# Kernel tuning notes

Hardware: AMD Instinct MI355X
Metric: run time of the kernel (lower is better)

## Reference

```python
import jax, jax.numpy as jnp
import numpy as np

B, D_IN, D_H, K, M = 4096, 512, 128, 16, 1250
N_GENES = K * M  # 20000


def setup_inputs() -> dict:
    key = jax.random.key(0)
    k_z, k_w1, k_w2 = jax.random.split(key, 3)
    z = jax.random.normal(k_z, (B, D_IN), dtype=jnp.float32)
    # Stacked parameters for the K identical-shape HydraHeads
    # (Linear(d_in, d_hidden) -> ReLU -> Linear(d_hidden, m_k)).
    W1 = jax.random.normal(k_w1, (K, D_IN, D_H), dtype=jnp.float32) / np.sqrt(D_IN)
    b1 = jnp.zeros((K, D_H), dtype=jnp.float32)
    W2 = jax.random.normal(k_w2, (K, D_H, M), dtype=jnp.float32) / np.sqrt(D_H)
    b2 = jnp.zeros((K, M), dtype=jnp.float32)
    # Strided canonical-order partition: head k owns genes k, k+K, k+2K, ...
    idx = jnp.arange(N_GENES, dtype=jnp.int32).reshape(M, K).T  # (K, M)
    return {"z": z, "W1": W1, "b1": b1, "W2": W2, "b2": b2, "idx": idx}


def reference(z, W1, b1, W2, b2, idx):
    # K small MLP heads, batched as one einsum pair instead of a Python loop.
    h = jax.nn.relu(jnp.einsum('bd,kdh->kbh', z, W1) + b1[:, None, :])   # (K, B, H)
    per_head = jnp.einsum('kbh,khm->kbm', h, W2) + b2[:, None, :]        # (K, B, M)
    # Scatter reassembly into registry-canonical order: full[:, idx[k]] = per_head[k]
    flat_idx = idx.reshape(-1)                                            # (K*M,)
    flat_heads = jnp.transpose(per_head, (1, 0, 2)).reshape(z.shape[0], K * M)
    full = jnp.zeros((z.shape[0], N_GENES), dtype=per_head.dtype)
    full = full.at[:, flat_idx].set(flat_heads)
    return full, per_head
```

## Files before the change

### kernel.cpp

```cpp
#include <hip/hip_runtime.h>


#define DEV static __device__ __forceinline__

typedef __attribute__((ext_vector_type(8))) short bf16x8;
typedef __attribute__((ext_vector_type(4))) float f32x4;
typedef __attribute__((ext_vector_type(4))) short s16x4;

constexpr int B = 4096, DIN = 512, DH = 128, K = 16, M = 1250, NG = K * M;
constexpr int MT = 32;
constexpr int NMT = (M + MT - 1) / MT;
constexpr int LDS_S = 516;

DEV unsigned short f2bf(float x) {
  unsigned u = __builtin_bit_cast(unsigned, x);
  u += 0x7FFFu + ((u >> 16) & 1u);
  return (unsigned short)(u >> 16);
}
DEV float bf2f(unsigned short b) {
  return __builtin_bit_cast(float, (unsigned)b << 16);
}
DEV void split_bf16(float x, short& hi, short& lo) {
  unsigned short h = f2bf(x);
  hi = (short)h;
  lo = (short)f2bf(x - bf2f(h));
}


__global__ __launch_bounds__(256)
void convert_all(const float* __restrict__ z, const float* __restrict__ w1,
                 const float* __restrict__ w2,
                 short* __restrict__ zhi, short* __restrict__ zlo,
                 short* __restrict__ w1hi, short* __restrict__ w1lo,
                 short* __restrict__ w2hi, short* __restrict__ w2lo) {
  const int g = blockIdx.x;
  if (g < 2048) {
    const int i = g * 256 + threadIdx.x;
    const float4 v = ((const float4*)z)[i];
    float vv[4] = {v.x, v.y, v.z, v.w};
    s16x4 h, l;
#pragma unroll
    for (int j = 0; j < 4; ++j) {
      unsigned short a = f2bf(vv[j]);
      h[j] = (short)a;
      l[j] = (short)f2bf(vv[j] - bf2f(a));
    }
    ((s16x4*)zhi)[i] = h;
    ((s16x4*)zlo)[i] = l;
  } else if (g < 6144) {
    const int n = (g - 2048) * 256 + threadIdx.x;
    const int d = n & (DIN - 1);
    const int h = (n >> 9) & (DH - 1);
    const int k = n >> 16;
    split_bf16(w1[(k * DIN + d) * DH + h], w1hi[n], w1lo[n]);
  } else {
    const int n = (g - 6144) * 256 + threadIdx.x;
    const int h = n & (DH - 1);
    const int t = n >> 7;
    const int m = t % M;
    const int k = t / M;
    split_bf16(w2[(k * DH + h) * M + m], w2hi[n], w2lo[n]);
  }
}


__global__ __launch_bounds__(256)
void gemm1(const short* __restrict__ zhi, const short* __restrict__ zlo,
           const short* __restrict__ w1hi, const short* __restrict__ w1lo,
           const float* __restrict__ b1,
           short* __restrict__ hhi, short* __restrict__ hlo) {
  const int lane = threadIdx.x & 63, wave = threadIdx.x >> 6;
  const int lr = lane & 15, lg = lane >> 4;
  const int g = blockIdx.x;
  const int w = (g & 7) * 128 + (g >> 3);
  const int k = w >> 6;
  const int b0 = (w & 63) * 64;
  const int c0 = wave * 32;

  f32x4 acc[4][2] = {};
  const short* w1hk = w1hi + k * DH * DIN;
  const short* w1lk = w1lo + k * DH * DIN;

  for (int kc = 0; kc < DIN; kc += 32) {
    const int ko = kc + lg * 8;
    bf16x8 bh[2], bl[2];
#pragma unroll
    for (int j = 0; j < 2; ++j) {
      const int off = (c0 + j * 16 + lr) * DIN + ko;
      bh[j] = *(const bf16x8*)(w1hk + off);
      bl[j] = *(const bf16x8*)(w1lk + off);
    }
#pragma unroll
    for (int i = 0; i < 4; ++i) {
      const int off = (b0 + i * 16 + lr) * DIN + ko;
      const bf16x8 ah = *(const bf16x8*)(zhi + off);
      const bf16x8 al = *(const bf16x8*)(zlo + off);
#pragma unroll
      for (int j = 0; j < 2; ++j) {
        acc[i][j] = __builtin_amdgcn_mfma_f32_16x16x32_bf16(ah, bh[j], acc[i][j], 0, 0, 0);
        acc[i][j] = __builtin_amdgcn_mfma_f32_16x16x32_bf16(ah, bl[j], acc[i][j], 0, 0, 0);
        acc[i][j] = __builtin_amdgcn_mfma_f32_16x16x32_bf16(al, bh[j], acc[i][j], 0, 0, 0);
      }
    }
  }

#pragma unroll
  for (int i = 0; i < 4; ++i) {
#pragma unroll
    for (int j = 0; j < 2; ++j) {
      const int col = c0 + j * 16 + lr;
      const float bias = b1[k * DH + col];
#pragma unroll
      for (int r = 0; r < 4; ++r) {
        const int row = b0 + i * 16 + lg * 4 + r;
        float v = acc[i][j][r] + bias;
        v = fmaxf(v, 0.f);
        short hi, lo;
        split_bf16(v, hi, lo);
        const int o = (k * B + row) * DH + col;
        hhi[o] = hi;
        hlo[o] = lo;
      }
    }
  }
}


__global__ __launch_bounds__(512)
void gemm2(const short* __restrict__ hhi, const short* __restrict__ hlo,
           const short* __restrict__ w2hi, const short* __restrict__ w2lo,
           const float* __restrict__ b2,
           float* __restrict__ full, float* __restrict__ ph) {
  const int tid = threadIdx.x;
  const int lane = tid & 63, wave = tid >> 6;
  const int lr = lane & 15, lg = lane >> 4;
  const int hgrp = wave & 3;
  const int mgrp = wave >> 2;
  const int g = blockIdx.x;
  const int w = (g & 7) * 320 + (g >> 3);
  const int bt = w / NMT;
  const int mt = w % NMT;
  const int b0 = bt * 64;
  const int m0 = mt * MT;
  const int mloc = mgrp * 16 + lr;
  const int mi = m0 + mloc;
  const int mc = mi < M ? mi : M - 1;
  const int khg = hgrp * 4;

  __shared__ __align__(16) float lds[16 * LDS_S];

  f32x4 acc[4][4] = {};

#pragma unroll
  for (int hk = 0; hk < 4; ++hk) {
    const int kh = khg + hk;
    const short* hh = hhi + ((long)(kh * B + b0)) * DH;
    const short* hl = hlo + ((long)(kh * B + b0)) * DH;
    const short* w2h = w2hi + (kh * M + mc) * DH;
    const short* w2l = w2lo + (kh * M + mc) * DH;
#pragma unroll
    for (int kc = 0; kc < DH; kc += 32) {
      const int ko = kc + lg * 8;
      const bf16x8 bh = *(const bf16x8*)(w2h + ko);
      const bf16x8 bl = *(const bf16x8*)(w2l + ko);
#pragma unroll
      for (int i = 0; i < 4; ++i) {
        const int offa = (i * 16 + lr) * DH + ko;
        const bf16x8 ah = *(const bf16x8*)(hh + offa);
        const bf16x8 al = *(const bf16x8*)(hl + offa);
        acc[hk][i] = __builtin_amdgcn_mfma_f32_16x16x32_bf16(ah, bh, acc[hk][i], 0, 0, 0);
        acc[hk][i] = __builtin_amdgcn_mfma_f32_16x16x32_bf16(ah, bl, acc[hk][i], 0, 0, 0);
        acc[hk][i] = __builtin_amdgcn_mfma_f32_16x16x32_bf16(al, bh, acc[hk][i], 0, 0, 0);
      }
    }
  }

  float bias[4];
#pragma unroll
  for (int hk = 0; hk < 4; ++hk) bias[hk] = b2[(khg + hk) * M + mc];

  const int Mrem = (M - m0 < MT) ? (M - m0) : MT;
  const int nf4 = Mrem * 4;
  const int wslot = (khg >> 2) + 0;

#pragma unroll
  for (int q = 0; q < 4; ++q) {
    __syncthreads();
#pragma unroll
    for (int r = 0; r < 4; ++r) {
      const int rowl = lg * 4 + r;
      f32x4 v;
#pragma unroll
      for (int hk = 0; hk < 4; ++hk) v[hk] = acc[hk][q][r] + bias[hk];
      const int slot = (wslot + mloc) & 3;
      *(f32x4*)&lds[rowl * LDS_S + mloc * 16 + slot * 4] = v;
      if (mi < M) {
        const int row = b0 + q * 16 + rowl;
        __builtin_nontemporal_store(v[0], &ph[((khg + 0) * B + row) * M + mi]);
        __builtin_nontemporal_store(v[1], &ph[((khg + 1) * B + row) * M + mi]);
        __builtin_nontemporal_store(v[2], &ph[((khg + 2) * B + row) * M + mi]);
        __builtin_nontemporal_store(v[3], &ph[((khg + 3) * B + row) * M + mi]);
      }
    }
    __syncthreads();
#pragma unroll
    for (int it = 0; it < 4; ++it) {
      const int f4id = it * 512 + tid;
      const int rowl = f4id >> 7;
      const int c4 = f4id & 127;
      if (c4 < nf4) {
        const int mg = c4 >> 2, s = c4 & 3;
        const int slot = (s + mg) & 3;
        const f32x4 v = *(const f32x4*)&lds[rowl * LDS_S + mg * 16 + slot * 4];
        __builtin_nontemporal_store(
            v, (f32x4*)&full[(b0 + q * 16 + rowl) * NG + m0 * 16 + c4 * 4]);
      }
    }
  }
}


extern "C" void kernel_launch(void* const* d_in, const int* in_sizes, int n_in,
                              void* d_out, int out_size, void* d_ws, size_t ws_size,
                              hipStream_t stream) {
  const float* z  = (const float*)d_in[0];
  const float* W1 = (const float*)d_in[1];
  const float* b1 = (const float*)d_in[2];
  const float* W2 = (const float*)d_in[3];
  const float* b2 = (const float*)d_in[4];

  short* ws = (short*)d_ws;
  const int ZN  = B * DIN;
  const int W1N = K * DIN * DH;
  const int W2N = K * DH * M;
  const int HN  = K * B * DH;
  short* zhi  = ws;           short* zlo  = zhi + ZN;
  short* w1hi = zlo + ZN;     short* w1lo = w1hi + W1N;
  short* w2hi = w1lo + W1N;   short* w2lo = w2hi + W2N;
  short* hhi  = w2lo + W2N;   short* hlo  = hhi + HN;

  float* full = (float*)d_out;
  float* ph   = full + (long)B * NG;

  convert_all<<<16144, 256, 0, stream>>>(z, W1, W2, zhi, zlo, w1hi, w1lo, w2hi, w2lo);
  gemm1<<<64 * K, 256, 0, stream>>>(zhi, zlo, w1hi, w1lo, b1, hhi, hlo);
  gemm2<<<NMT * 64, 512, 0, stream>>>(hhi, hlo, w2hi, w2lo, b2, full, ph);
}
```

Measured before the change: 1.246 ms.

## Stage gemm2 operands through double-buffered LDS with direct global-to-LDS loads

gemm2 now walks the 16 heads sequentially, using global_load_lds to copy swizzled H and W2 tiles into a double-buffered LDS ring. Each stage is prefetched while the MFMAs of the previous stage run, replacing per-lane direct global loads. The wave decomposition changes from head-groups to batch-quarters by M halves, so each wave holds 16 accumulators. The block mapping also becomes M-tile-major. This adds a large dynamic LDS footprint and more barriers, which may limit occupancy, and drops nontemporal stores for the per-head output.

After: 1.050 ms. 15.7% less time.

```diff
diff --git a/kernel.cpp b/kernel.cpp
--- a/kernel.cpp
+++ b/kernel.cpp
@@ -6,11 +6,15 @@
 typedef __attribute__((ext_vector_type(8))) short bf16x8;
 typedef __attribute__((ext_vector_type(4))) float f32x4;
 typedef __attribute__((ext_vector_type(4))) short s16x4;
+typedef unsigned int u32;
 
 constexpr int B = 4096, DIN = 512, DH = 128, K = 16, M = 1250, NG = K * M;
-constexpr int MT = 32;
-constexpr int NMT = (M + MT - 1) / MT;
+constexpr int MT = 32, NMT = 40;
 constexpr int LDS_S = 516;
+constexpr int HBUF = 0;
+constexpr int WBUF = 65536;
+constexpr int PANEL = 98304;
+constexpr int LDS_TOTAL = PANEL + 16 * LDS_S * 4;
 
 DEV unsigned short f2bf(float x) {
   unsigned u = __builtin_bit_cast(unsigned, x);
@@ -24,6 +28,11 @@
   unsigned short h = f2bf(x);
   hi = (short)h;
   lo = (short)f2bf(x - bf2f(h));
+}
+DEV void dma16(const void* g, void* l) {
+  __builtin_amdgcn_global_load_lds(
+      (const __attribute__((address_space(1))) u32*)g,
+      (__attribute__((address_space(3))) u32*)l, 16, 0, 0);
 }
 
 
@@ -126,94 +135,155 @@
 }
 
 
-__global__ __launch_bounds__(512)
+__global__ __launch_bounds__(512, 2)
 void gemm2(const short* __restrict__ hhi, const short* __restrict__ hlo,
            const short* __restrict__ w2hi, const short* __restrict__ w2lo,
            const float* __restrict__ b2,
            float* __restrict__ full, float* __restrict__ ph) {
+  extern __shared__ char smem[];
   const int tid = threadIdx.x;
   const int lane = tid & 63, wave = tid >> 6;
   const int lr = lane & 15, lg = lane >> 4;
-  const int hgrp = wave & 3;
-  const int mgrp = wave >> 2;
+  const int bq = wave >> 1, mg = wave & 1;
   const int g = blockIdx.x;
   const int w = (g & 7) * 320 + (g >> 3);
-  const int bt = w / NMT;
-  const int mt = w % NMT;
-  const int b0 = bt * 64;
-  const int m0 = mt * MT;
-  const int mloc = mgrp * 16 + lr;
+  const int mt = w / 64;
+  const int bt = w % 64;
+  const int b0 = bt * 64, m0 = mt * MT;
+
+  const short* gp[6];
+  int ls0[6], ls1[6];
+  long stride[6];
+#pragma unroll
+  for (int c6 = 0; c6 < 6; ++c6) {
+    const int id = wave + c6 * 8;
+    if (id < 16) {
+      const int c = id;
+      const int row = c * 4 + (lane >> 4);
+      const int sg = (lane & 15) ^ (row & 7);
+      gp[c6] = hhi + (long)(b0 + row) * DH + sg * 8;
+      ls0[c6] = HBUF + c * 1024;
+      ls1[c6] = HBUF + 32768 + c * 1024;
+      stride[c6] = (long)B * DH;
+    } else if (id < 32) {
+      const int c = id - 16;
+      const int row = c * 4 + (lane >> 4);
+      const int sg = (lane & 15) ^ (row & 7);
+      gp[c6] = hlo + (long)(b0 + row) * DH + sg * 8;
+      ls0[c6] = HBUF + 16384 + c * 1024;
+      ls1[c6] = HBUF + 32768 + 16384 + c * 1024;
+      stride[c6] = (long)B * DH;
+    } else if (id < 40) {
+      const int c = id - 32;
+      const int row = c * 4 + (lane >> 4);
+      const int sg = (lane & 15) ^ (row & 7);
+      gp[c6] = w2hi + (long)(m0 + row) * DH + sg * 8;
+      ls0[c6] = WBUF + c * 1024;
+      ls1[c6] = WBUF + 16384 + c * 1024;
+      stride[c6] = (long)M * DH;
+    } else {
+      const int c = id - 40;
+      const int row = c * 4 + (lane >> 4);
+      const int sg = (lane & 15) ^ (row & 7);
+      gp[c6] = w2lo + (long)(m0 + row) * DH + sg * 8;
+      ls0[c6] = WBUF + 8192 + c * 1024;
+      ls1[c6] = WBUF + 16384 + 8192 + c * 1024;
+      stride[c6] = (long)M * DH;
+    }
+  }
+
+#define ISSUE(PAR)                                                  \
+  do {                                                              \
+    _Pragma("unroll") for (int c6 = 0; c6 < 6; ++c6)                \
+        dma16(gp[c6], smem + ((PAR) ? ls1[c6] : ls0[c6]));          \
+  } while (0)
+#define ADV()                                                       \
+  do {                                                              \
+    _Pragma("unroll") for (int c6 = 0; c6 < 6; ++c6)                \
+        gp[c6] += stride[c6];                                       \
+  } while (0)
+
+  f32x4 acc[16] = {};
+  const int arow = bq * 16 + lr;
+  const int mrow = mg * 16 + lr;
+
+  ISSUE(0);
+#pragma unroll
+  for (int p = 0; p < 16; ++p) {
+    if (p < 15) {
+      ADV();
+      if ((p + 1) & 1) ISSUE(1); else ISSUE(0);
+      asm volatile("s_waitcnt vmcnt(6)" ::: "memory");
+    } else {
+      asm volatile("s_waitcnt vmcnt(0)" ::: "memory");
+    }
+    __builtin_amdgcn_sched_barrier(0);
+    __builtin_amdgcn_s_barrier();
+    __builtin_amdgcn_sched_barrier(0);
+    const char* hb = smem + HBUF + ((p & 1) ? 32768 : 0);
+    const char* wb = smem + WBUF + ((p & 1) ? 16384 : 0);
+#pragma unroll
+    for (int s = 0; s < 4; ++s) {
+      const int gx = (((s * 4 + lg) ^ (lr & 7))) * 16;
+      const bf16x8 ah = *(const bf16x8*)(hb + arow * 256 + gx);
+      const bf16x8 al = *(const bf16x8*)(hb + 16384 + arow * 256 + gx);
+      const bf16x8 bh = *(const bf16x8*)(wb + mrow * 256 + gx);
+      const bf16x8 bl = *(const bf16x8*)(wb + 8192 + mrow * 256 + gx);
+      acc[p] = __builtin_amdgcn_mfma_f32_16x16x32_bf16(ah, bh, acc[p], 0, 0, 0);
+      acc[p] = __builtin_amdgcn_mfma_f32_16x16x32_bf16(ah, bl, acc[p], 0, 0, 0);
+      acc[p] = __builtin_amdgcn_mfma_f32_16x16x32_bf16(al, bh, acc[p], 0, 0, 0);
+    }
+    __builtin_amdgcn_sched_barrier(0);
+    __builtin_amdgcn_s_barrier();
+    __builtin_amdgcn_sched_barrier(0);
+  }
+#undef ISSUE
+#undef ADV
+
+  float* panel = (float*)(smem + PANEL);
+  const int mloc = mg * 16 + lr;
   const int mi = m0 + mloc;
-  const int mc = mi < M ? mi : M - 1;
-  const int khg = hgrp * 4;
-
-  __shared__ __align__(16) float lds[16 * LDS_S];
-
-  f32x4 acc[4][4] = {};
-
-#pragma unroll
-  for (int hk = 0; hk < 4; ++hk) {
-    const int kh = khg + hk;
-    const short* hh = hhi + ((long)(kh * B + b0)) * DH;
-    const short* hl = hlo + ((long)(kh * B + b0)) * DH;
-    const short* w2h = w2hi + (kh * M + mc) * DH;
-    const short* w2l = w2lo + (kh * M + mc) * DH;
-#pragma unroll
-    for (int kc = 0; kc < DH; kc += 32) {
-      const int ko = kc + lg * 8;
-      const bf16x8 bh = *(const bf16x8*)(w2h + ko);
-      const bf16x8 bl = *(const bf16x8*)(w2l + ko);
-#pragma unroll
-      for (int i = 0; i < 4; ++i) {
-        const int offa = (i * 16 + lr) * DH + ko;
-        const bf16x8 ah = *(const bf16x8*)(hh + offa);
-        const bf16x8 al = *(const bf16x8*)(hl + offa);
-        acc[hk][i] = __builtin_amdgcn_mfma_f32_16x16x32_bf16(ah, bh, acc[hk][i], 0, 0, 0);
-        acc[hk][i] = __builtin_amdgcn_mfma_f32_16x16x32_bf16(ah, bl, acc[hk][i], 0, 0, 0);
-        acc[hk][i] = __builtin_amdgcn_mfma_f32_16x16x32_bf16(al, bh, acc[hk][i], 0, 0, 0);
-      }
-    }
-  }
-
-  float bias[4];
-#pragma unroll
-  for (int hk = 0; hk < 4; ++hk) bias[hk] = b2[(khg + hk) * M + mc];
-
+  const int mc2 = mi < M ? mi : M - 1;
+  float bias[16];
+#pragma unroll
+  for (int kh = 0; kh < 16; ++kh) bias[kh] = b2[kh * M + mc2];
   const int Mrem = (M - m0 < MT) ? (M - m0) : MT;
   const int nf4 = Mrem * 4;
-  const int wslot = (khg >> 2) + 0;
 
 #pragma unroll
   for (int q = 0; q < 4; ++q) {
     __syncthreads();
-#pragma unroll
-    for (int r = 0; r < 4; ++r) {
-      const int rowl = lg * 4 + r;
-      f32x4 v;
-#pragma unroll
-      for (int hk = 0; hk < 4; ++hk) v[hk] = acc[hk][q][r] + bias[hk];
-      const int slot = (wslot + mloc) & 3;
-      *(f32x4*)&lds[rowl * LDS_S + mloc * 16 + slot * 4] = v;
-      if (mi < M) {
-        const int row = b0 + q * 16 + rowl;
-        __builtin_nontemporal_store(v[0], &ph[((khg + 0) * B + row) * M + mi]);
-        __builtin_nontemporal_store(v[1], &ph[((khg + 1) * B + row) * M + mi]);
-        __builtin_nontemporal_store(v[2], &ph[((khg + 2) * B + row) * M + mi]);
-        __builtin_nontemporal_store(v[3], &ph[((khg + 3) * B + row) * M + mi]);
+    if (bq == q) {
+#pragma unroll
+      for (int r = 0; r < 4; ++r) {
+        const int rowl = lg * 4 + r;
+        const int grow = b0 + q * 16 + rowl;
+#pragma unroll
+        for (int hg = 0; hg < 4; ++hg) {
+          f32x4 v;
+#pragma unroll
+          for (int j = 0; j < 4; ++j) v[j] = acc[hg * 4 + j][r] + bias[hg * 4 + j];
+          const int slot = (hg + (mloc >> 1)) & 3;
+          *(f32x4*)&panel[rowl * LDS_S + mloc * 16 + slot * 4] = v;
+          if (mi < M) {
+#pragma unroll
+            for (int j = 0; j < 4; ++j)
+              ph[((long)(hg * 4 + j) * B + grow) * M + mi] = v[j];
+          }
+        }
       }
     }
     __syncthreads();
 #pragma unroll
     for (int it = 0; it < 4; ++it) {
       const int f4id = it * 512 + tid;
-      const int rowl = f4id >> 7;
-      const int c4 = f4id & 127;
+      const int rowl = f4id >> 7, c4 = f4id & 127;
       if (c4 < nf4) {
-        const int mg = c4 >> 2, s = c4 & 3;
-        const int slot = (s + mg) & 3;
-        const f32x4 v = *(const f32x4*)&lds[rowl * LDS_S + mg * 16 + slot * 4];
+        const int pm = c4 >> 2, hg = c4 & 3;
+        const int slot = (hg + (pm >> 1)) & 3;
+        const f32x4 v = *(const f32x4*)&panel[rowl * LDS_S + pm * 16 + slot * 4];
         __builtin_nontemporal_store(
-            v, (f32x4*)&full[(b0 + q * 16 + rowl) * NG + m0 * 16 + c4 * 4]);
+            v, (f32x4*)&full[(long)(b0 + q * 16 + rowl) * NG + m0 * 16 + c4 * 4]);
       }
     }
   }
@@ -242,7 +312,10 @@
   float* full = (float*)d_out;
   float* ph   = full + (long)B * NG;
 
+  hipFuncSetAttribute((const void*)gemm2,
+                      hipFuncAttributeMaxDynamicSharedMemorySize, LDS_TOTAL);
+
   convert_all<<<16144, 256, 0, stream>>>(z, W1, W2, zhi, zlo, w1hi, w1lo, w2hi, w2lo);
   gemm1<<<64 * K, 256, 0, stream>>>(zhi, zlo, w1hi, w1lo, b1, hhi, hlo);
-  gemm2<<<NMT * 64, 512, 0, stream>>>(hhi, hlo, w2hi, w2lo, b2, full, ph);
-}
+  gemm2<<<NMT * 64, 512, LDS_TOTAL, stream>>>(hhi, hlo, w2hi, w2lo, b2, full, ph);
+}
```
